# Optimization experiments

Measured on AMD Instinct MI355X. Metric: run time of the kernel, lower is better.

## Reference

```python
import jax, jax.numpy as jnp
import numpy as np

STEPS = 2
P_TOPP = 0.9
TAU = 1.0
LN_EPS = 1e-5


def _top_p_attention(pooled, W1, W2, W3):
    # pooled: (N, C). Bilinear scores -> softmax -> nucleus (top-p) sparsify -> renorm.
    e1 = pooled @ W1.T                      # (N, d)
    e3 = pooled @ W3.T                      # (N, d)
    logits = (e1 @ W2.T) @ e3.T / TAU       # (N, N)
    attn = jax.nn.softmax(logits, axis=-1)
    srt = jnp.sort(attn, axis=-1)[:, ::-1]  # descending
    csum = jnp.cumsum(srt, axis=-1)
    keep = (csum - srt) < P_TOPP            # keep entries whose exclusive cum-prob < p
    thr = jnp.min(jnp.where(keep, srt, jnp.inf), axis=-1, keepdims=True)
    masked = jnp.where(attn >= thr, attn, 0.0)
    return masked / jnp.clip(jnp.sum(masked, axis=-1, keepdims=True), 1e-12)


def _layernorm(h, gamma, beta):
    mu = jnp.mean(h, axis=-1, keepdims=True)
    var = jnp.mean(jnp.square(h - mu), axis=-1, keepdims=True)
    return (h - mu) * jax.lax.rsqrt(var + LN_EPS) * gamma + beta


def _forward(x, prior, W1, W2, W3, prior_fwd_w, adaptive_w, ln_gamma, ln_beta, alpha):
    # Row-normalised prior (forward diffusion operator)
    Rf = prior / jnp.clip(jnp.sum(prior, axis=1, keepdims=True), 1e-12)
    Xf = x
    Xa = x
    residual = jnp.zeros_like(x)
    for idx in range(STEPS):
        pooled = jnp.mean(Xa, axis=1)                      # protein axis pooling -> (N_P, C)
        attn = _top_p_attention(pooled, W1, W2, W3)        # (N_P, N_P)
        Xf = jnp.einsum('ij,jkc->ikc', Rf, Xf)
        Xa = jnp.einsum('ij,jkc->ikc', attn, Xa)
        delta = jnp.einsum('ikc,dc->ikd', Xf, prior_fwd_w[idx]) \
              + jnp.einsum('ikc,dc->ikd', Xa, adaptive_w[idx])
        residual = residual + delta                        # dropout is identity in eval mode
    gate = jax.nn.sigmoid(alpha)                           # (1,)
    return _layernorm(x + gate * residual, ln_gamma, ln_beta)


def setup_inputs() -> dict:
    key = jax.random.key(0)
    ks = jax.random.split(key, 8)
    N_P, N_C, C, D = 2048, 64, 128, 64
    x = jax.random.normal(ks[0], (N_P, N_C, C), dtype=jnp.float32)
    prior = jax.random.uniform(ks[1], (N_P, N_P), dtype=jnp.float32)
    W1 = jax.random.normal(ks[2], (D, C), dtype=jnp.float32) / np.sqrt(C)
    W2 = jax.random.normal(ks[3], (D, D), dtype=jnp.float32) / np.sqrt(D)
    W3 = jax.random.normal(ks[4], (D, C), dtype=jnp.float32) / np.sqrt(C)
    prior_fwd_w = jax.random.normal(ks[5], (STEPS, C, C), dtype=jnp.float32) / np.sqrt(C)
    adaptive_w = jax.random.normal(ks[6], (STEPS, C, C), dtype=jnp.float32) / np.sqrt(C)
    ln_gamma = jnp.ones((C,), dtype=jnp.float32)
    ln_beta = jnp.zeros((C,), dtype=jnp.float32)
    alpha = jnp.zeros((1,), dtype=jnp.float32)
    return {"x": x, "prior": prior, "W1": W1, "W2": W2, "W3": W3,
            "prior_fwd_w": prior_fwd_w, "adaptive_w": adaptive_w,
            "ln_gamma": ln_gamma, "ln_beta": ln_beta, "alpha": alpha}


def reference(x, prior, W1, W2, W3, prior_fwd_w, adaptive_w, ln_gamma, ln_beta, alpha):
    return _forward(x, prior, W1, W2, W3, prior_fwd_w, adaptive_w, ln_gamma, ln_beta, alpha)
```

## Files before the change

kernel.cpp:

```cpp
#include <hip/hip_runtime.h>

typedef unsigned short u16;
typedef __attribute__((ext_vector_type(8))) short short8;
typedef __attribute__((ext_vector_type(4))) float f32x4;
typedef __attribute__((ext_vector_type(16))) float f32x16;

#define AS1 __attribute__((address_space(1)))
#define AS3 __attribute__((address_space(3)))

__device__ __forceinline__ void async_cp16(const void* g, void* l) {
  __builtin_amdgcn_global_load_lds((const AS1 unsigned int*)g, (AS3 unsigned int*)l, 16, 0, 0);
}

__device__ __forceinline__ u16 f2bf(float f) {
  union { float f; unsigned u; } v; v.f = f;
  unsigned r = v.u + 0x7fffu + ((v.u >> 16) & 1u);
  return (u16)(r >> 16);
}
__device__ __forceinline__ float bf2f(u16 h) {
  union { unsigned u; float f; } v; v.u = ((unsigned)h) << 16;
  return v.f;
}

template<int MODE>
__global__ __launch_bounds__(512, 2) void gemm32(
    const u16* __restrict__ A, const u16* __restrict__ B,
    int M, int N, int K,
    u16* __restrict__ Crow, int crow_ld, int crow_coloff,
    u16* __restrict__ Ct, int ct_ld)
{
  extern __shared__ u16 smem[];
  const int tid  = threadIdx.x;
  const int lane = tid & 63;
  const int w    = tid >> 6;
  const int m0 = blockIdx.y * 256;
  const int n0 = blockIdx.x * 256;
  const int wm = w >> 2;
  const int wn = w & 3;
  const int l31  = lane & 31;
  const int half = lane >> 5;
  const int pl   = (l31 & 3) ^ ((l31 >> 2) & 3);

  f32x16 acc[4][2];
#pragma unroll
  for (int i = 0; i < 4; i++)
#pragma unroll
    for (int j = 0; j < 2; j++)
#pragma unroll
      for (int r = 0; r < 16; r++) acc[i][j][r] = 0.f;

  const int sr4 = lane >> 2, sc4 = lane & 3;
  const int pp  = (sr4 & 3) ^ (sr4 >> 2);
  const int gko = (sc4 ^ pp) * 8;
  const u16* gA0 = A + (size_t)(m0 + w * 32 + sr4) * K + gko;
  const u16* gA1 = A + (size_t)(m0 + w * 32 + 16 + sr4) * K + gko;
  const u16* gB0 = B + (size_t)(n0 + w * 32 + sr4) * K + gko;
  const u16* gB1 = B + (size_t)(n0 + w * 32 + 16 + sr4) * K + gko;
  const int la = w * 1024;

#define ISSUE(tt) do {                                       \
    u16* sa = smem + ((tt) & 3) * 16384 + la;                \
    u16* sb = sa + 8192;                                     \
    const int ko = (tt) * 32;                                \
    async_cp16(gA0 + ko, sa); async_cp16(gA1 + ko, sa + 512);\
    async_cp16(gB0 + ko, sb); async_cp16(gB1 + ko, sb + 512);\
  } while (0)

  const int NT = K >> 5;
  ISSUE(0); ISSUE(1);
  asm volatile("s_waitcnt vmcnt(4)" ::: "memory");
  __builtin_amdgcn_s_barrier();

  for (int t = 0; t < NT; ++t) {
    const u16* sAp = smem + (t & 3) * 16384;
    const u16* sBp = sAp + 8192;
    const bool st = (t + 2 < NT);
    if (st) ISSUE(t + 2);

    const int ar = (wm * 128 + l31) * 32;
    const int br = (wn * 64 + l31) * 32;
    short8 Af[4][2], Bf[2][2];
#define FRAG(ks) ((((ks) * 2 + half) ^ pl) * 8)
#pragma unroll
    for (int i = 0; i < 4; i++)
#pragma unroll
      for (int ks = 0; ks < 2; ks++)
        Af[i][ks] = *(const short8*)(sAp + ar + i * 1024 + FRAG(ks));
#pragma unroll
    for (int j = 0; j < 2; j++)
#pragma unroll
      for (int ks = 0; ks < 2; ks++)
        Bf[j][ks] = *(const short8*)(sBp + br + j * 1024 + FRAG(ks));
#undef FRAG

    __builtin_amdgcn_s_setprio(1);
#pragma unroll
    for (int i = 0; i < 4; i++)
#pragma unroll
      for (int j = 0; j < 2; j++)
#pragma unroll
        for (int ks = 0; ks < 2; ks++)
          acc[i][j] = __builtin_amdgcn_mfma_f32_32x32x16_bf16(Af[i][ks], Bf[j][ks], acc[i][j], 0, 0, 0);
    __builtin_amdgcn_s_setprio(0);

    if (st) { asm volatile("s_waitcnt vmcnt(4)" ::: "memory"); }
    else    { asm volatile("s_waitcnt vmcnt(0)" ::: "memory"); }
    __builtin_amdgcn_s_barrier();
  }
#undef ISSUE

  u16* T = smem;

#pragma unroll
  for (int pr = 0; pr < 4; pr++) {
    if (wm == (pr >> 1)) {
#pragma unroll
      for (int ii = 0; ii < 2; ii++)
#pragma unroll
        for (int j = 0; j < 2; j++)
#pragma unroll
          for (int r = 0; r < 16; r++) {
            const int rloc = ii * 32 + (r & 3) + 8 * (r >> 2) + 4 * half;
            T[rloc * 264 + wn * 64 + j * 32 + l31] = f2bf(acc[(pr & 1) * 2 + ii][j][r]);
          }
    }
    __syncthreads();
    {
      const int row = tid >> 3, c8 = tid & 7;
      const size_t grow = (size_t)(m0 + pr * 64 + row);
      const size_t crow = grow * (size_t)(N >> 7) + (n0 >> 7) + (c8 >> 2);
      u16* dst = Crow + crow * (size_t)crow_ld + crow_coloff + (c8 & 3) * 32;
      const u16* src = T + row * 264 + c8 * 32;
#pragma unroll
      for (int u = 0; u < 4; u++) ((float4*)dst)[u] = ((const float4*)src)[u];
    }
    __syncthreads();
  }

  if constexpr (MODE == 1) {
#pragma unroll
    for (int p = 0; p < 4; p++) {
      if (wn == p) {
#pragma unroll
        for (int i = 0; i < 4; i++)
#pragma unroll
          for (int j = 0; j < 2; j++)
#pragma unroll
            for (int r = 0; r < 16; r++) {
              const int nloc = j * 32 + l31;
              const int mcol = wm * 128 + i * 32 + (r & 3) + 8 * (r >> 2) + 4 * half;
              T[nloc * 264 + mcol] = f2bf(acc[i][j][r]);
            }
      }
      __syncthreads();
      {
        const int row = tid >> 3, c8 = tid & 7;
        u16* dst = Ct + (size_t)(n0 + p * 64 + row) * ct_ld + m0 + c8 * 32;
        const u16* src = T + row * 264 + c8 * 32;
#pragma unroll
        for (int u = 0; u < 4; u++) ((float4*)dst)[u] = ((const float4*)src)[u];
      }
      __syncthreads();
    }
  }
}

template<int MODE>
__global__ __launch_bounds__(256) void gemm_bt(
    const u16* __restrict__ A, const u16* __restrict__ B,
    int M, int N, int K,
    float* __restrict__ Cf,
    u16* __restrict__ Crow, int crow_ld, int crow_coloff)
{
  extern __shared__ char smemc[];
  u16* sA = (u16*)smemc;
  u16* sB = (u16*)(smemc + 8192);
  const int tid  = threadIdx.x;
  const int lane = tid & 63;
  const int wid  = tid >> 6;
  const int m0 = blockIdx.y * 128;
  const int n0 = blockIdx.x * 128;
  const int wm = (wid >> 1) * 64;
  const int wn = (wid & 1) * 64;
  const int ml = lane & 15;
  const int qd = lane >> 4;

  f32x4 acc[4][4];
  const f32x4 zero = {0.f, 0.f, 0.f, 0.f};
#pragma unroll
  for (int i = 0; i < 4; i++)
#pragma unroll
    for (int j = 0; j < 4; j++) acc[i][j] = zero;

  const int r4 = tid >> 2;
  const int c4 = (tid & 3) * 8;
  const u16* gA0 = A + (size_t)(m0 + r4) * K + c4;
  const u16* gA1 = A + (size_t)(m0 + 64 + r4) * K + c4;
  const u16* gB0 = B + (size_t)(n0 + r4) * K + c4;
  const u16* gB1 = B + (size_t)(n0 + 64 + r4) * K + c4;
  u16* lA0 = sA + wid * 512;
  u16* lA1 = sA + 2048 + wid * 512;
  u16* lB0 = sB + wid * 512;
  u16* lB1 = sB + 2048 + wid * 512;

  for (int k0 = 0; k0 < K; k0 += 32) {
    async_cp16(gA0 + k0, lA0);
    async_cp16(gA1 + k0, lA1);
    async_cp16(gB0 + k0, lB0);
    async_cp16(gB1 + k0, lB1);
    __syncthreads();
    short8 af[4], bfr[4];
#pragma unroll
    for (int i = 0; i < 4; i++)
      af[i] = *(const short8*)(sA + (wm + i * 16 + ml) * 32 + qd * 8);
#pragma unroll
    for (int j = 0; j < 4; j++)
      bfr[j] = *(const short8*)(sB + (wn + j * 16 + ml) * 32 + qd * 8);
#pragma unroll
    for (int i = 0; i < 4; i++)
#pragma unroll
      for (int j = 0; j < 4; j++)
        acc[i][j] = __builtin_amdgcn_mfma_f32_16x16x32_bf16(af[i], bfr[j], acc[i][j], 0, 0, 0);
    __syncthreads();
  }

  if constexpr (MODE == 3) {
#pragma unroll
    for (int i = 0; i < 4; i++) {
      const int mr = m0 + wm + i * 16 + qd * 4;
#pragma unroll
      for (int j = 0; j < 4; j++) {
        const int nc = n0 + wn + j * 16 + ml;
        float* p = Cf + (size_t)mr * N + nc;
#pragma unroll
        for (int r = 0; r < 4; r++) p[(size_t)r * N] = acc[i][j][r];
      }
    }
  } else {
    u16* T = (u16*)smemc;
#pragma unroll
    for (int i = 0; i < 4; i++)
#pragma unroll
      for (int j = 0; j < 4; j++)
#pragma unroll
        for (int r = 0; r < 4; r++)
          T[(wm + i * 16 + qd * 4 + r) * 136 + wn + j * 16 + ml] = f2bf(acc[i][j][r]);
    __syncthreads();
    const int row = tid >> 1, halfr = tid & 1;
    const size_t crow = (size_t)(m0 + row) * (N >> 7) + (n0 >> 7);
    u16* dst = Crow + crow * (size_t)crow_ld + crow_coloff + halfr * 64;
    const u16* src = T + row * 136 + halfr * 64;
#pragma unroll
    for (int u = 0; u < 8; u++) ((float4*)dst)[u] = ((const float4*)src)[u];
  }
}

__global__ void rowsum_k(const float* __restrict__ prior, float* __restrict__ rs) {
  const int i = blockIdx.x, t = threadIdx.x;
  const float* p = prior + (size_t)i * 2048;
  float s = 0.f;
  for (int j = t; j < 2048; j += 256) s += p[j];
  __shared__ float red[256];
  red[t] = s; __syncthreads();
  for (int o = 128; o; o >>= 1) { if (t < o) red[t] += red[t + o]; __syncthreads(); }
  if (t == 0) rs[i] = red[0];
}

__global__ void convprior_k(const float4* __restrict__ prior, const float* __restrict__ rs,
                            ushort4* __restrict__ dst) {
  const int idx = blockIdx.x * 256 + threadIdx.x;
  const float inv = 1.0f / rs[idx >> 9];
  const float4 v = prior[idx];
  ushort4 o;
  o.x = f2bf(v.x * inv); o.y = f2bf(v.y * inv); o.z = f2bf(v.z * inv); o.w = f2bf(v.w * inv);
  dst[idx] = o;
}

__global__ void convx_k(const float* __restrict__ x, u16* __restrict__ xt) {
  __shared__ float S[64][65];
  const int t = threadIdx.x;
  const int j0 = blockIdx.y * 64;
  const int n0 = blockIdx.x * 64;
  const int rr = t >> 4, cxc = (t & 15) * 4;
#pragma unroll
  for (int p = 0; p < 4; p++) {
    const float4 v = *(const float4*)(x + (size_t)(j0 + rr + p * 16) * 8192 + n0 + cxc);
    S[rr + p * 16][cxc + 0] = v.x; S[rr + p * 16][cxc + 1] = v.y;
    S[rr + p * 16][cxc + 2] = v.z; S[rr + p * 16][cxc + 3] = v.w;
  }
  __syncthreads();
  const int nl = t >> 2, ch = (t & 3) * 16;
  alignas(16) u16 tmp[16];
#pragma unroll
  for (int u = 0; u < 16; u++) tmp[u] = f2bf(S[ch + u][nl]);
  float4* dst = (float4*)(xt + (size_t)(n0 + nl) * 2048 + j0 + ch);
  dst[0] = ((const float4*)tmp)[0];
  dst[1] = ((const float4*)tmp)[1];
}

__global__ void convw_k(const float* __restrict__ pw, const float* __restrict__ aw,
                        u16* __restrict__ btc) {
  const int idx = blockIdx.x * 256 + threadIdx.x;
  const int k = idx & 255, d = (idx >> 8) & 127, s = idx >> 15;
  const float v = (k < 128) ? aw[(s * 128 + d) * 128 + k] : pw[(s * 128 + d) * 128 + (k - 128)];
  btc[idx] = f2bf(v);
}

__global__ void pooled1_k(const float* __restrict__ x, float* __restrict__ pooled) {
  const int i = blockIdx.x, t = threadIdx.x;
  const int c = t & 127, h = t >> 7;
  const float* base = x + (size_t)i * 8192 + c;
  float s = 0.f;
  for (int k = h * 32; k < h * 32 + 32; k++) s += base[(size_t)k * 128];
  __shared__ float red[256];
  red[t] = s; __syncthreads();
  if (t < 128) pooled[i * 128 + t] = (red[t] + red[t + 128]) * (1.f / 64.f);
}

__global__ void pooled2_k(const u16* __restrict__ comb, float* __restrict__ pooled) {
  const int i = blockIdx.x, t = threadIdx.x;
  const int c = t & 127, h = t >> 7;
  const u16* base = comb + (size_t)i * 64 * 256 + c;
  float s = 0.f;
  for (int k = h * 32; k < h * 32 + 32; k++) s += bf2f(base[(size_t)k * 256]);
  __shared__ float red[256];
  red[t] = s; __syncthreads();
  if (t < 128) pooled[i * 128 + t] = (red[t] + red[t + 128]) * (1.f / 64.f);
}

__global__ void epre_k(const float* __restrict__ pooled,
                       const float* __restrict__ W1, const float* __restrict__ W2,
                       const float* __restrict__ W3,
                       u16* __restrict__ e3b, u16* __restrict__ fb) {
  const int i = blockIdx.x, d = threadIdx.x;
  __shared__ float pr[128], e1s[64];
  pr[d] = pooled[i * 128 + d];
  pr[d + 64] = pooled[i * 128 + 64 + d];
  __syncthreads();
  float s1 = 0.f, s3 = 0.f;
  for (int c = 0; c < 128; c++) {
    const float p = pr[c];
    s1 += p * W1[d * 128 + c];
    s3 += p * W3[d * 128 + c];
  }
  e1s[d] = s1;
  e3b[i * 64 + d] = f2bf(s3);
  __syncthreads();
  float sf = 0.f;
  for (int dd = 0; dd < 64; dd++) sf += e1s[dd] * W2[d * 64 + dd];
  fb[i * 64 + d] = f2bf(sf);
}

__device__ __forceinline__ float waveRedSum(float v) {
#pragma unroll
  for (int o = 1; o < 64; o <<= 1) v += __shfl_xor(v, o);
  return __shfl(v, 0);
}
__device__ __forceinline__ float waveRedMax(float v) {
#pragma unroll
  for (int o = 1; o < 64; o <<= 1) v = fmaxf(v, __shfl_xor(v, o));
  return __shfl(v, 0);
}

__global__ __launch_bounds__(256) void topp_k(const float* __restrict__ logits,
                                              u16* __restrict__ attnb) {
  const int w = threadIdx.x >> 6, l = threadIdx.x & 63;
  const int i = blockIdx.x * 4 + w;
  const float4* row = (const float4*)(logits + (size_t)i * 2048);
  float E[32];
  float mx = -1e30f;
#pragma unroll
  for (int k = 0; k < 8; k++) {
    const float4 v = row[k * 64 + l];
    E[k * 4 + 0] = v.x; E[k * 4 + 1] = v.y; E[k * 4 + 2] = v.z; E[k * 4 + 3] = v.w;
    mx = fmaxf(fmaxf(mx, fmaxf(v.x, v.y)), fmaxf(v.z, v.w));
  }
  mx = waveRedMax(mx);
  float S = 0.f;
#pragma unroll
  for (int u = 0; u < 32; u++) { E[u] = __expf(E[u] - mx); S += E[u]; }
  S = waveRedSum(S);
  const float target = 0.9f * S;
  float lo = 0.f, hi = 1.f;
  for (int it = 0; it < 32; ++it) {
    const float mid = 0.5f * (lo + hi);
    float g = 0.f;
#pragma unroll
    for (int u = 0; u < 32; u++) g += (E[u] > mid) ? E[u] : 0.f;
    g = waveRedSum(g);
    const bool below = (g < target);
    hi = below ? mid : hi;
    lo = below ? lo : mid;
  }
  float Sk = 0.f;
#pragma unroll
  for (int u = 0; u < 32; u++) Sk += (E[u] > lo) ? E[u] : 0.f;
  Sk = waveRedSum(Sk);
  const float inv = 1.f / Sk;
  u16* dst = attnb + (size_t)i * 2048;
#pragma unroll
  for (int k = 0; k < 8; k++) {
    ushort4 o;
    o.x = f2bf(E[k * 4 + 0] > lo ? E[k * 4 + 0] * inv : 0.f);
    o.y = f2bf(E[k * 4 + 1] > lo ? E[k * 4 + 1] * inv : 0.f);
    o.z = f2bf(E[k * 4 + 2] > lo ? E[k * 4 + 2] * inv : 0.f);
    o.w = f2bf(E[k * 4 + 3] > lo ? E[k * 4 + 3] * inv : 0.f);
    *(ushort4*)(dst + k * 256 + l * 4) = o;
  }
}

__global__ void ln_k(const float* __restrict__ x,
                     const u16* __restrict__ d1, const u16* __restrict__ d2,
                     float* __restrict__ out,
                     const float* __restrict__ gamma, const float* __restrict__ beta,
                     const float* __restrict__ alpha) {
  const int wid = threadIdx.x >> 6, lane = threadIdx.x & 63;
  const float gate = 1.f / (1.f + expf(-alpha[0]));
  const float2 g = ((const float2*)gamma)[lane];
  const float2 b = ((const float2*)beta)[lane];
#pragma unroll
  for (int rr = 0; rr < 2; ++rr) {
    const size_t row = (size_t)blockIdx.x * 8 + wid * 2 + rr;
    const float2 xv = ((const float2*)(x + row * 128))[lane];
    const ushort2 r1 = ((const ushort2*)(d1 + row * 128))[lane];
    const ushort2 r2 = ((const ushort2*)(d2 + row * 128))[lane];
    const float h0 = xv.x + gate * (bf2f(r1.x) + bf2f(r2.x));
    const float h1 = xv.y + gate * (bf2f(r1.y) + bf2f(r2.y));
    float s = h0 + h1;
#pragma unroll
    for (int o = 32; o; o >>= 1) s += __shfl_down(s, o);
    const float mu = __shfl(s, 0) * (1.f / 128.f);
    const float d0 = h0 - mu, dd1 = h1 - mu;
    float vs = d0 * d0 + dd1 * dd1;
#pragma unroll
    for (int o = 32; o; o >>= 1) vs += __shfl_down(vs, o);
    const float rstd = rsqrtf(__shfl(vs, 0) * (1.f / 128.f) + 1e-5f);
    float2* op = (float2*)(out + row * 128);
    float2 ov;
    ov.x = d0 * rstd * g.x + b.x;
    ov.y = dd1 * rstd * g.y + b.y;
    op[lane] = ov;
  }
}

extern "C" void kernel_launch(void* const* d_in, const int* in_sizes, int n_in,
                              void* d_out, int out_size, void* d_ws, size_t ws_size,
                              hipStream_t stream) {
  const float* x     = (const float*)d_in[0];
  const float* prior = (const float*)d_in[1];
  const float* W1    = (const float*)d_in[2];
  const float* W2    = (const float*)d_in[3];
  const float* W3    = (const float*)d_in[4];
  const float* Pw    = (const float*)d_in[5];
  const float* Aw    = (const float*)d_in[6];
  const float* gamma = (const float*)d_in[7];
  const float* beta  = (const float*)d_in[8];
  const float* alpha = (const float*)d_in[9];
  float* out = (float*)d_out;

  char* w = (char*)d_ws;
  u16*   Xt_x   = (u16*)(w);
  u16*   XtA    = (u16*)(w + 33554432);
  u16*   XtF    = (u16*)(w + 67108864);
  u16*   comb   = (u16*)(w + 100663296);
  u16*   priorS = (u16*)(w + 167772160);
  u16*   attnb  = (u16*)(w + 176160768);
  float* pooled = (float*)(w + 184549376);
  u16*   e3b    = (u16*)(w + 185597952);
  u16*   fb     = (u16*)(w + 186122240);
  float* rs     = (float*)(w + 186646528);
  u16*   btc    = (u16*)(w + 186654720);
  float* logits1 = (float*)(w + 33554432);
  float* logits2 = (float*)(w);
  u16*   d1      = (u16*)(w);
  u16*   d2      = (u16*)(w + 33554432);
  (void)in_sizes; (void)n_in; (void)ws_size;

  static bool attr_done = false;
  if (!attr_done) {
    hipFuncSetAttribute(reinterpret_cast<const void*>(gemm32<1>),
                        hipFuncAttributeMaxDynamicSharedMemorySize, 131072);
    hipFuncSetAttribute(reinterpret_cast<const void*>(gemm32<2>),
                        hipFuncAttributeMaxDynamicSharedMemorySize, 131072);
    attr_done = true;
  }

  rowsum_k   <<<2048, 256, 0, stream>>>(prior, rs);
  convprior_k<<<4096, 256, 0, stream>>>((const float4*)prior, rs, (ushort4*)priorS);
  convx_k    <<<dim3(128, 32), 256, 0, stream>>>(x, Xt_x);
  convw_k    <<<256, 256, 0, stream>>>(Pw, Aw, btc);

  pooled1_k  <<<2048, 256, 0, stream>>>(x, pooled);
  epre_k     <<<2048, 64, 0, stream>>>(pooled, W1, W2, W3, e3b, fb);
  gemm_bt<3> <<<dim3(16, 16), 256, 16384, stream>>>(fb, e3b, 2048, 2048, 64,
                                                    logits1, nullptr, 0, 0);
  topp_k     <<<512, 256, 0, stream>>>(logits1, attnb);

  gemm32<1><<<dim3(32, 8), 512, 131072, stream>>>(attnb,  Xt_x, 2048, 8192, 2048,
                                                  comb, 256, 0,   XtA, 2048);
  gemm32<1><<<dim3(32, 8), 512, 131072, stream>>>(priorS, Xt_x, 2048, 8192, 2048,
                                                  comb, 256, 128, XtF, 2048);

  pooled2_k  <<<2048, 256, 0, stream>>>(comb, pooled);
  epre_k     <<<2048, 64, 0, stream>>>(pooled, W1, W2, W3, e3b, fb);
  gemm_bt<3> <<<dim3(16, 16), 256, 16384, stream>>>(fb, e3b, 2048, 2048, 64,
                                                    logits2, nullptr, 0, 0);
  topp_k     <<<512, 256, 0, stream>>>(logits2, attnb);

  gemm_bt<2><<<dim3(1, 1024), 256, 34816, stream>>>(comb, btc, 131072, 128, 256,
                                                    nullptr, d1, 128, 0);

  gemm32<2><<<dim3(32, 8), 512, 131072, stream>>>(attnb,  XtA, 2048, 8192, 2048,
                                                  comb, 256, 0,   nullptr, 0);
  gemm32<2><<<dim3(32, 8), 512, 131072, stream>>>(priorS, XtF, 2048, 8192, 2048,
                                                  comb, 256, 128, nullptr, 0);

  gemm_bt<2><<<dim3(1, 1024), 256, 34816, stream>>>(comb, btc + 32768, 131072, 128, 256,
                                                    nullptr, d2, 128, 0);

  ln_k<<<16384, 256, 0, stream>>>(x, d1, d2, out, gamma, beta, alpha);
}
```

Measured before the change: 646.1 us.

## Deepen global prefetch to three stages and ping-pong LDS fragment registers

The GEMM main loop now keeps three K-tiles of global-to-LDS async copies in flight instead of two, using the existing 4-slot LDS ring. LDS fragment reads are split into two half-K register sets that alternate (P/Q), so the next fragments load while MFMAs run on the current set. The single barrier moves to the top of the loop. The aim is to hide memory and LDS latency behind matrix-core work, at the cost of more live registers, which may lower occupancy.

New measurement: 657.9 us. Within noise of the previous version (+1.8%).

```diff
diff --git a/kernel.cpp b/kernel.cpp
--- a/kernel.cpp
+++ b/kernel.cpp
@@ -67,46 +67,52 @@
   } while (0)
 
   const int NT = K >> 5;
-  ISSUE(0); ISSUE(1);
-  asm volatile("s_waitcnt vmcnt(4)" ::: "memory");
+  ISSUE(0); ISSUE(1); ISSUE(2);
+  asm volatile("s_waitcnt vmcnt(8)" ::: "memory");
   __builtin_amdgcn_s_barrier();
 
+  const int ar = (wm * 128 + l31) * 32;
+  const int br = (wn * 64 + l31) * 32;
+#define FRAG(ks) ((((ks) * 2 + half) ^ pl) * 8)
+#define READF(R, ss) do {                                                   \
+    const u16* sp_ = smem + (((ss) >> 1) & 3) * 16384;                      \
+    const int kc_ = FRAG((ss) & 1);                                         \
+    R##A[0] = *(const short8*)(sp_ + ar +    0 + kc_);                      \
+    R##A[1] = *(const short8*)(sp_ + ar + 1024 + kc_);                      \
+    R##A[2] = *(const short8*)(sp_ + ar + 2048 + kc_);                      \
+    R##A[3] = *(const short8*)(sp_ + ar + 3072 + kc_);                      \
+    R##B[0] = *(const short8*)(sp_ + 8192 + br +    0 + kc_);               \
+    R##B[1] = *(const short8*)(sp_ + 8192 + br + 1024 + kc_);               \
+  } while (0)
+#define MFMAC(R) do {                                                      \
+    __builtin_amdgcn_s_setprio(1);                                         \
+    _Pragma("unroll")                                                      \
+    for (int i_ = 0; i_ < 4; i_++)                                         \
+      _Pragma("unroll")                                                    \
+      for (int j_ = 0; j_ < 2; j_++)                                       \
+        acc[i_][j_] = __builtin_amdgcn_mfma_f32_32x32x16_bf16(             \
+            R##A[i_], R##B[j_], acc[i_][j_], 0, 0, 0);                     \
+    __builtin_amdgcn_s_setprio(0);                                         \
+  } while (0)
+
+  short8 PA[4], PB[2], QA[4], QB[2];
+  READF(P, 0);
+
   for (int t = 0; t < NT; ++t) {
-    const u16* sAp = smem + (t & 3) * 16384;
-    const u16* sBp = sAp + 8192;
-    const bool st = (t + 2 < NT);
-    if (st) ISSUE(t + 2);
-
-    const int ar = (wm * 128 + l31) * 32;
-    const int br = (wn * 64 + l31) * 32;
-    short8 Af[4][2], Bf[2][2];
-#define FRAG(ks) ((((ks) * 2 + half) ^ pl) * 8)
-#pragma unroll
-    for (int i = 0; i < 4; i++)
-#pragma unroll
-      for (int ks = 0; ks < 2; ks++)
-        Af[i][ks] = *(const short8*)(sAp + ar + i * 1024 + FRAG(ks));
-#pragma unroll
-    for (int j = 0; j < 2; j++)
-#pragma unroll
-      for (int ks = 0; ks < 2; ks++)
-        Bf[j][ks] = *(const short8*)(sBp + br + j * 1024 + FRAG(ks));
+    if (t + 2 < NT) { asm volatile("s_waitcnt vmcnt(4)" ::: "memory"); }
+    else            { asm volatile("s_waitcnt vmcnt(0)" ::: "memory"); }
+    __builtin_amdgcn_s_barrier();
+    if (t + 3 < NT) ISSUE(t + 3);
+
+    READF(Q, 2 * t + 1);
+    MFMAC(P);
+    if (t + 1 < NT) READF(P, 2 * t + 2);
+    MFMAC(Q);
+  }
+  __syncthreads();
+#undef READF
+#undef MFMAC
 #undef FRAG
-
-    __builtin_amdgcn_s_setprio(1);
-#pragma unroll
-    for (int i = 0; i < 4; i++)
-#pragma unroll
-      for (int j = 0; j < 2; j++)
-#pragma unroll
-        for (int ks = 0; ks < 2; ks++)
-          acc[i][j] = __builtin_amdgcn_mfma_f32_32x32x16_bf16(Af[i][ks], Bf[j][ks], acc[i][j], 0, 0, 0);
-    __builtin_amdgcn_s_setprio(0);
-
-    if (st) { asm volatile("s_waitcnt vmcnt(4)" ::: "memory"); }
-    else    { asm volatile("s_waitcnt vmcnt(0)" ::: "memory"); }
-    __builtin_amdgcn_s_barrier();
-  }
 #undef ISSUE
 
   u16* T = smem;
```
